# Kernel tuning notes

Hardware: AMD Instinct MI355X
Metric: run time of the kernel (lower is better)

The kernel has to match this reference:

```python
import jax, jax.numpy as jnp
import numpy as np

N_NODES = 100000
HIDDEN = 128
N_EDGES = 1000000


def setup_inputs() -> dict:
    key = jax.random.key(0)
    k1, k2, k3 = jax.random.split(key, 3)
    z = jax.random.normal(k1, (N_NODES, HIDDEN), dtype=jnp.float32)
    edge_index = jax.random.randint(k2, (2, N_EDGES), 0, N_NODES, dtype=jnp.int64)
    # xavier_uniform for square matrix: bound = sqrt(6/(fan_in+fan_out))
    bound = float(np.sqrt(6.0 / (HIDDEN + HIDDEN)))
    weights = jax.random.uniform(k3, (HIDDEN, HIDDEN), dtype=jnp.float32,
                                 minval=-bound, maxval=bound)
    return {"z": z, "edge_index": edge_index, "weights": weights}


def reference(z, edge_index, weights):
    # symm=True: symmetrize the bilinear form
    W = weights + weights.T                      # [d, d]
    z_src = z[edge_index[0]]                     # [E, d] gather
    z_dst = z[edge_index[1]]                     # [E, d] gather
    # torch: (W @ z_dst.T).T == z_dst @ W.T
    value = jnp.einsum('ed,dk,ek->e', z_src, W, z_dst)  # row-wise bilinear score
    return jax.nn.sigmoid(value)
```

## Files before the change

kernel.cpp:

```cpp
#include <hip/hip_runtime.h>

#define HIDDEN 128
#define LDSW 136
#define BSHIFT 10
#define NBMAX 128
#define CAP 10752
#define OVF_MAX 65536

typedef _Float16 f16;
typedef f16 f16x2 __attribute__((ext_vector_type(2)));
typedef f16 f16x8 __attribute__((ext_vector_type(8)));
typedef float f32x16 __attribute__((ext_vector_type(16)));
typedef unsigned long long ull;

static __device__ __forceinline__ float fdot2(f16x2 a, f16x2 b, float c) {
    return __builtin_amdgcn_fdot2(a, b, c, false);
}

__global__ __launch_bounds__(256) void prep_w(const float* __restrict__ w,
                                              f16* __restrict__ wsh_t,
                                              int* __restrict__ cursor,
                                              int* __restrict__ ovf_cnt) {
    int idx = blockIdx.x * 256 + threadIdx.x;
    if (idx < NBMAX) cursor[idx] = idx * CAP;
    if (idx == NBMAX) ovf_cnt[0] = 0;
    int n = idx >> 7, k = idx & 127;
    wsh_t[idx] = (f16)(w[k * HIDDEN + n] + w[n * HIDDEN + k]);
}

__global__ __launch_bounds__(256) void gemm_scatter(const float* __restrict__ z,
                                                    const f16* __restrict__ wsh_t,
                                                    f16* __restrict__ zh,
                                                    f16* __restrict__ uh,
                                                    const int* __restrict__ eidx,
                                                    int* __restrict__ cursor,
                                                    ull* __restrict__ perm,
                                                    ull* __restrict__ ovf,
                                                    int* __restrict__ ovf_cnt,
                                                    int nrows, int E, int nb, int ngemm) {
    __shared__ f16 wlt[HIDDEN * LDSW];
    int tid = threadIdx.x;

    if (blockIdx.x >= ngemm) {
        int* lh    = (int*)wlt;
        int* lbase = lh + NBMAX;
        int* lrank = lbase + NBMAX;
        int base = (blockIdx.x - ngemm) * 4096;
        if (tid < NBMAX) { lh[tid] = 0; lrank[tid] = 0; }
        __syncthreads();
        int s[16], d[16], bb[16];
        #pragma unroll
        for (int i = 0; i < 16; ++i) {
            int e = base + i * 256 + tid;
            bb[i] = -1;
            if (e < E) {
                s[i] = eidx[e]; d[i] = eidx[E + e];
                bb[i] = d[i] >> BSHIFT;
                atomicAdd(&lh[bb[i]], 1);
            }
        }
        __syncthreads();
        if (tid < nb && lh[tid]) lbase[tid] = atomicAdd(&cursor[tid], lh[tid]);
        __syncthreads();
        #pragma unroll
        for (int i = 0; i < 16; ++i) {
            if (bb[i] >= 0) {
                int e = base + i * 256 + tid;
                int r = atomicAdd(&lrank[bb[i]], 1);
                long pos = (long)lbase[bb[i]] + r;
                ull v = (ull)s[i] | ((ull)d[i] << 17) | ((ull)e << 34);
                if (pos < (long)(bb[i] + 1) * CAP) perm[pos] = v;
                else {
                    int o = atomicAdd(ovf_cnt, 1);
                    if (o < OVF_MAX) ovf[o] = v;
                }
            }
        }
        return;
    }

    {
        const f16x8* g = (const f16x8*)wsh_t;
        #pragma unroll
        for (int it = 0; it < 8; ++it) {
            int idx = it * 256 + tid;
            int j = idx >> 4, kc = idx & 15;
            *(f16x8*)&wlt[j * LDSW + kc * 8] = g[idx];
        }
    }
    __syncthreads();

    int wave = tid >> 6, lane = tid & 63;
    int row0 = blockIdx.x * 128 + wave * 32;
    if (row0 > nrows - 32) row0 = nrows - 32;

    int m = lane & 31, half = lane >> 5;
    const float* zr = z  + (size_t)(row0 + m) * HIDDEN + half * 8;
    f16*        zhr = zh + (size_t)(row0 + m) * HIDDEN + half * 8;
    const f16* wbase = &wlt[m * LDSW + half * 8];

    f32x16 acc0, acc1, acc2, acc3;
    #pragma unroll
    for (int r = 0; r < 16; ++r) { acc0[r] = 0.f; acc1[r] = 0.f; acc2[r] = 0.f; acc3[r] = 0.f; }

    #pragma unroll
    for (int ks = 0; ks < 8; ++ks) {
        float4 a0 = *(const float4*)(zr + 16 * ks);
        float4 a1 = *(const float4*)(zr + 16 * ks + 4);
        f16x8 af = {(f16)a0.x, (f16)a0.y, (f16)a0.z, (f16)a0.w,
                    (f16)a1.x, (f16)a1.y, (f16)a1.z, (f16)a1.w};
        *(f16x8*)(zhr + 16 * ks) = af;
        f16x8 b0 = *(const f16x8*)(wbase + 16 * ks);
        f16x8 b1 = *(const f16x8*)(wbase + 32 * LDSW + 16 * ks);
        f16x8 b2 = *(const f16x8*)(wbase + 64 * LDSW + 16 * ks);
        f16x8 b3 = *(const f16x8*)(wbase + 96 * LDSW + 16 * ks);
        acc0 = __builtin_amdgcn_mfma_f32_32x32x16_f16(af, b0, acc0, 0, 0, 0);
        acc1 = __builtin_amdgcn_mfma_f32_32x32x16_f16(af, b1, acc1, 0, 0, 0);
        acc2 = __builtin_amdgcn_mfma_f32_32x32x16_f16(af, b2, acc2, 0, 0, 0);
        acc3 = __builtin_amdgcn_mfma_f32_32x32x16_f16(af, b3, acc3, 0, 0, 0);
    }

    f16* ur = uh + (size_t)row0 * HIDDEN;
    #pragma unroll
    for (int r = 0; r < 16; ++r) {
        int row = (r & 3) + 8 * (r >> 2) + 4 * half;
        f16* p = ur + (size_t)row * HIDDEN + m;
        p[0]  = (f16)acc0[r];
        p[32] = (f16)acc1[r];
        p[64] = (f16)acc2[r];
        p[96] = (f16)acc3[r];
    }
}

static __device__ __forceinline__ void score_edge(const f16* uh, const f16* zh,
                                                  ull p, float* out, int t, int E) {
    int src = (int)(p & 0x1FFFF);
    int dst = (int)((p >> 17) & 0x1FFFF);
    int eid = (int)(p >> 34);
    const float4* a4 = (const float4*)(uh + (size_t)src * HIDDEN);
    const float4* b4 = (const float4*)(zh + (size_t)dst * HIDDEN);
    float4 av = a4[t], bv = b4[t];
    const f16x2* ap = (const f16x2*)&av;
    const f16x2* bp = (const f16x2*)&bv;
    float s = 0.f;
    #pragma unroll
    for (int i = 0; i < 4; ++i) s = fdot2(ap[i], bp[i], s);
    #pragma unroll
    for (int off = 8; off > 0; off >>= 1) s += __shfl_down(s, off, 16);
    if (t == 0 && eid < E) out[eid] = 1.0f / (1.0f + __expf(-s));
}

__global__ __launch_bounds__(256) void edge_bin(const f16* __restrict__ uh,
                                                const f16* __restrict__ zh,
                                                const ull* __restrict__ perm,
                                                const ull* __restrict__ ovf,
                                                const int* __restrict__ ovf_cnt,
                                                float* __restrict__ out,
                                                int E, int cpx, int nmain) {
    int tid = threadIdx.x;
    int g = tid >> 4, t = tid & 15;
    int b = blockIdx.x;
    if (b >= nmain) {
        int n = ovf_cnt[0];
        if (n > OVF_MAX) n = OVF_MAX;
        for (int i = (b - nmain) * 16 + g; i < n; i += 32 * 16)
            score_edge(uh, zh, ovf[i], out, t, E);
        return;
    }
    int chunk = (b & 7) * cpx + (b >> 3);
    long slot = (long)chunk * 16 + g;
    score_edge(uh, zh, perm[slot], out, t, E);
}

__global__ __launch_bounds__(256) void edge_score16(const f16* __restrict__ uh,
                                                    const f16* __restrict__ zh,
                                                    const int* __restrict__ eidx,
                                                    float* __restrict__ out, int E) {
    int tid = threadIdx.x;
    int g = tid >> 4, t = tid & 15;
    int e = blockIdx.x * 16 + g;
    if (e >= E) return;
    ull p = (ull)eidx[e] | ((ull)eidx[E + e] << 17) | ((ull)e << 34);
    score_edge(uh, zh, p, out, t, E);
}

extern "C" void kernel_launch(void* const* d_in, const int* in_sizes, int n_in,
                              void* d_out, int out_size, void* d_ws, size_t ws_size,
                              hipStream_t stream) {
    const float* z    = (const float*)d_in[0];
    const int*   eidx = (const int*)d_in[1];
    const float* w    = (const float*)d_in[2];
    float* out = (float*)d_out;

    int nrows = in_sizes[0] / HIDDEN;
    int E = out_size;
    int nb = (nrows >> BSHIFT) + 1;

    f16* wsh_t  = (f16*)d_ws;
    f16* zh     = wsh_t + HIDDEN * HIDDEN;
    f16* uh     = zh + (size_t)nrows * HIDDEN;
    int* cursor = (int*)(uh + (size_t)nrows * HIDDEN);
    int* ovf_cnt = cursor + NBMAX;
    ull* ovf    = (ull*)(ovf_cnt + 2);
    ull* perm   = ovf + OVF_MAX;

    long nslots = (long)nb * CAP;
    size_t need = (size_t)((char*)(perm + nslots) - (char*)d_ws);
    bool binned = ws_size >= need;

    int ngemm = (nrows + 127) / 128;
    int nscat = (E + 4095) / 4096;

    prep_w<<<64, 256, 0, stream>>>(w, wsh_t, cursor, ovf_cnt);
    if (binned) {
        gemm_scatter<<<ngemm + nscat, 256, 0, stream>>>(z, wsh_t, zh, uh, eidx, cursor,
                                                        perm, ovf, ovf_cnt, nrows, E, nb, ngemm);
        long ngrp = nslots / 16;
        int cpx = (int)(ngrp / 8);
        int nmain = (int)ngrp;
        edge_bin<<<nmain + 32, 256, 0, stream>>>(uh, zh, perm, ovf, ovf_cnt, out, E, cpx, nmain);
    } else {
        gemm_scatter<<<ngemm, 256, 0, stream>>>(z, wsh_t, zh, uh, eidx, cursor,
                                                perm, ovf, ovf_cnt, nrows, E, nb, ngemm);
        edge_score16<<<(E + 15) / 16, 256, 0, stream>>>(uh, zh, eidx, out, E);
    }
}
```

Baseline: 165.9 us.

## Use fine-grained 32-row destination bins with one block per bin

Shrinks the destination bins from 1024 rows to 32 rows, giving about 3.1k bins of 448 slots each. Each bin is now scored by a single 1024-thread block that loops over its slots, with bins spread across XCD-interleaved block indices. The goal is to keep each bin's small destination row set hot in cache during the gathers. In exchange, every scatter block does far more global cursor atomics and LDS histogram initialisation, and each bin's unused padding slots are still processed.

New measurement: 178.4 us. 1.08x slower.

```diff
diff --git a/kernel.cpp b/kernel.cpp
--- a/kernel.cpp
+++ b/kernel.cpp
@@ -2,10 +2,10 @@
 
 #define HIDDEN 128
 #define LDSW 136
-#define BSHIFT 10
-#define NBMAX 128
-#define CAP 10752
-#define OVF_MAX 65536
+#define BSHIFT 5
+#define NBMAX 3136
+#define CAP 448
+#define OVF_MAX 16384
 
 typedef _Float16 f16;
 typedef f16 f16x2 __attribute__((ext_vector_type(2)));
@@ -20,10 +20,11 @@
 __global__ __launch_bounds__(256) void prep_w(const float* __restrict__ w,
                                               f16* __restrict__ wsh_t,
                                               int* __restrict__ cursor,
-                                              int* __restrict__ ovf_cnt) {
+                                              int* __restrict__ ovf_cnt,
+                                              int nb) {
     int idx = blockIdx.x * 256 + threadIdx.x;
-    if (idx < NBMAX) cursor[idx] = idx * CAP;
-    if (idx == NBMAX) ovf_cnt[0] = 0;
+    if (idx < nb) cursor[idx] = idx * CAP;
+    if (idx == nb) ovf_cnt[0] = 0;
     int n = idx >> 7, k = idx & 127;
     wsh_t[idx] = (f16)(w[k * HIDDEN + n] + w[n * HIDDEN + k]);
 }
@@ -38,15 +39,15 @@
                                                     ull* __restrict__ ovf,
                                                     int* __restrict__ ovf_cnt,
                                                     int nrows, int E, int nb, int ngemm) {
-    __shared__ f16 wlt[HIDDEN * LDSW];
+    __shared__ __align__(16) char smem[3 * NBMAX * 4];
     int tid = threadIdx.x;
 
     if (blockIdx.x >= ngemm) {
-        int* lh    = (int*)wlt;
+        int* lh    = (int*)smem;
         int* lbase = lh + NBMAX;
         int* lrank = lbase + NBMAX;
         int base = (blockIdx.x - ngemm) * 4096;
-        if (tid < NBMAX) { lh[tid] = 0; lrank[tid] = 0; }
+        for (int i = tid; i < nb; i += 256) { lh[i] = 0; lrank[i] = 0; }
         __syncthreads();
         int s[16], d[16], bb[16];
         #pragma unroll
@@ -60,7 +61,8 @@
             }
         }
         __syncthreads();
-        if (tid < nb && lh[tid]) lbase[tid] = atomicAdd(&cursor[tid], lh[tid]);
+        for (int i = tid; i < nb; i += 256)
+            if (lh[i]) lbase[i] = atomicAdd(&cursor[i], lh[i]);
         __syncthreads();
         #pragma unroll
         for (int i = 0; i < 16; ++i) {
@@ -79,6 +81,7 @@
         return;
     }
 
+    f16* wlt = (f16*)smem;
     {
         const f16x8* g = (const f16x8*)wsh_t;
         #pragma unroll
@@ -150,26 +153,29 @@
     if (t == 0 && eid < E) out[eid] = 1.0f / (1.0f + __expf(-s));
 }
 
-__global__ __launch_bounds__(256) void edge_bin(const f16* __restrict__ uh,
-                                                const f16* __restrict__ zh,
-                                                const ull* __restrict__ perm,
-                                                const ull* __restrict__ ovf,
-                                                const int* __restrict__ ovf_cnt,
-                                                float* __restrict__ out,
-                                                int E, int cpx, int nmain) {
+__global__ __launch_bounds__(1024) void edge_bin(const f16* __restrict__ uh,
+                                                 const f16* __restrict__ zh,
+                                                 const ull* __restrict__ perm,
+                                                 const ull* __restrict__ ovf,
+                                                 const int* __restrict__ ovf_cnt,
+                                                 float* __restrict__ out,
+                                                 int E, int cpb, int nb, int nmain) {
     int tid = threadIdx.x;
     int g = tid >> 4, t = tid & 15;
     int b = blockIdx.x;
     if (b >= nmain) {
         int n = ovf_cnt[0];
         if (n > OVF_MAX) n = OVF_MAX;
-        for (int i = (b - nmain) * 16 + g; i < n; i += 32 * 16)
+        for (int i = (b - nmain) * 64 + g; i < n; i += 32 * 64)
             score_edge(uh, zh, ovf[i], out, t, E);
         return;
     }
-    int chunk = (b & 7) * cpx + (b >> 3);
-    long slot = (long)chunk * 16 + g;
-    score_edge(uh, zh, perm[slot], out, t, E);
+    int B = (b & 7) * cpb + (b >> 3);
+    if (B >= nb) return;
+    long base = (long)B * CAP;
+    #pragma unroll 2
+    for (int j = 0; j < CAP / 64; ++j)
+        score_edge(uh, zh, perm[base + (long)j * 64 + g], out, t, E);
 }
 
 __global__ __launch_bounds__(256) void edge_score16(const f16* __restrict__ uh,
@@ -194,7 +200,7 @@
 
     int nrows = in_sizes[0] / HIDDEN;
     int E = out_size;
-    int nb = (nrows >> BSHIFT) + 1;
+    int nb = ((nrows - 1) >> BSHIFT) + 1;
 
     f16* wsh_t  = (f16*)d_ws;
     f16* zh     = wsh_t + HIDDEN * HIDDEN;
@@ -211,14 +217,14 @@
     int ngemm = (nrows + 127) / 128;
     int nscat = (E + 4095) / 4096;
 
-    prep_w<<<64, 256, 0, stream>>>(w, wsh_t, cursor, ovf_cnt);
+    prep_w<<<64, 256, 0, stream>>>(w, wsh_t, cursor, ovf_cnt, nb);
     if (binned) {
         gemm_scatter<<<ngemm + nscat, 256, 0, stream>>>(z, wsh_t, zh, uh, eidx, cursor,
                                                         perm, ovf, ovf_cnt, nrows, E, nb, ngemm);
-        long ngrp = nslots / 16;
-        int cpx = (int)(ngrp / 8);
-        int nmain = (int)ngrp;
-        edge_bin<<<nmain + 32, 256, 0, stream>>>(uh, zh, perm, ovf, ovf_cnt, out, E, cpx, nmain);
+        int cpb = (nb + 7) / 8;
+        int nmain = 8 * cpb;
+        edge_bin<<<nmain + 32, 1024, 0, stream>>>(uh, zh, perm, ovf, ovf_cnt, out,
+                                                  E, cpb, nb, nmain);
     } else {
         gemm_scatter<<<ngemm, 256, 0, stream>>>(z, wsh_t, zh, uh, eidx, cursor,
                                                 perm, ovf, ovf_cnt, nrows, E, nb, ngemm);
```

## Drop LDS staging of W and split GEMM output columns across waves

Applied to the files above, without the earlier changes.

The GEMM part no longer copies the 128x128 f16 weight matrix into shared memory. Each block now handles 32 rows, and each of its four waves computes one 32-column slice, reading W fragments straight from global memory, which should mostly hit cache. Removing the large LDS allocation and adding a minimum-occupancy launch bound should allow more resident blocks and give the fused scatter blocks more room. The cost is four times more GEMM blocks, each wave reloading the z rows, and W being read from global/L2 instead of LDS.

After: 200.5 us. +20.9%, slower.

```diff
diff --git a/kernel.cpp b/kernel.cpp
--- a/kernel.cpp
+++ b/kernel.cpp
@@ -1,7 +1,6 @@
 #include <hip/hip_runtime.h>
 
 #define HIDDEN 128
-#define LDSW 136
 #define BSHIFT 10
 #define NBMAX 128
 #define CAP 10752
@@ -28,23 +27,20 @@
     wsh_t[idx] = (f16)(w[k * HIDDEN + n] + w[n * HIDDEN + k]);
 }
 
-__global__ __launch_bounds__(256) void gemm_scatter(const float* __restrict__ z,
-                                                    const f16* __restrict__ wsh_t,
-                                                    f16* __restrict__ zh,
-                                                    f16* __restrict__ uh,
-                                                    const int* __restrict__ eidx,
-                                                    int* __restrict__ cursor,
-                                                    ull* __restrict__ perm,
-                                                    ull* __restrict__ ovf,
-                                                    int* __restrict__ ovf_cnt,
-                                                    int nrows, int E, int nb, int ngemm) {
-    __shared__ f16 wlt[HIDDEN * LDSW];
+__global__ __launch_bounds__(256, 6) void gemm_scatter(const float* __restrict__ z,
+                                                       const f16* __restrict__ wsh_t,
+                                                       f16* __restrict__ zh,
+                                                       f16* __restrict__ uh,
+                                                       const int* __restrict__ eidx,
+                                                       int* __restrict__ cursor,
+                                                       ull* __restrict__ perm,
+                                                       ull* __restrict__ ovf,
+                                                       int* __restrict__ ovf_cnt,
+                                                       int nrows, int E, int nb, int ngemm) {
     int tid = threadIdx.x;
 
     if (blockIdx.x >= ngemm) {
-        int* lh    = (int*)wlt;
-        int* lbase = lh + NBMAX;
-        int* lrank = lbase + NBMAX;
+        __shared__ int lh[NBMAX], lbase[NBMAX], lrank[NBMAX];
         int base = (blockIdx.x - ngemm) * 4096;
         if (tid < NBMAX) { lh[tid] = 0; lrank[tid] = 0; }
         __syncthreads();
@@ -79,29 +75,18 @@
         return;
     }
 
-    {
-        const f16x8* g = (const f16x8*)wsh_t;
-        #pragma unroll
-        for (int it = 0; it < 8; ++it) {
-            int idx = it * 256 + tid;
-            int j = idx >> 4, kc = idx & 15;
-            *(f16x8*)&wlt[j * LDSW + kc * 8] = g[idx];
-        }
-    }
-    __syncthreads();
-
     int wave = tid >> 6, lane = tid & 63;
-    int row0 = blockIdx.x * 128 + wave * 32;
+    int row0 = blockIdx.x * 32;
     if (row0 > nrows - 32) row0 = nrows - 32;
 
     int m = lane & 31, half = lane >> 5;
     const float* zr = z  + (size_t)(row0 + m) * HIDDEN + half * 8;
     f16*        zhr = zh + (size_t)(row0 + m) * HIDDEN + half * 8;
-    const f16* wbase = &wlt[m * LDSW + half * 8];
-
-    f32x16 acc0, acc1, acc2, acc3;
-    #pragma unroll
-    for (int r = 0; r < 16; ++r) { acc0[r] = 0.f; acc1[r] = 0.f; acc2[r] = 0.f; acc3[r] = 0.f; }
+    const f16* wb = wsh_t + (size_t)(32 * wave + m) * HIDDEN + half * 8;
+
+    f32x16 acc;
+    #pragma unroll
+    for (int r = 0; r < 16; ++r) acc[r] = 0.f;
 
     #pragma unroll
     for (int ks = 0; ks < 8; ++ks) {
@@ -109,26 +94,16 @@
         float4 a1 = *(const float4*)(zr + 16 * ks + 4);
         f16x8 af = {(f16)a0.x, (f16)a0.y, (f16)a0.z, (f16)a0.w,
                     (f16)a1.x, (f16)a1.y, (f16)a1.z, (f16)a1.w};
-        *(f16x8*)(zhr + 16 * ks) = af;
-        f16x8 b0 = *(const f16x8*)(wbase + 16 * ks);
-        f16x8 b1 = *(const f16x8*)(wbase + 32 * LDSW + 16 * ks);
-        f16x8 b2 = *(const f16x8*)(wbase + 64 * LDSW + 16 * ks);
-        f16x8 b3 = *(const f16x8*)(wbase + 96 * LDSW + 16 * ks);
-        acc0 = __builtin_amdgcn_mfma_f32_32x32x16_f16(af, b0, acc0, 0, 0, 0);
-        acc1 = __builtin_amdgcn_mfma_f32_32x32x16_f16(af, b1, acc1, 0, 0, 0);
-        acc2 = __builtin_amdgcn_mfma_f32_32x32x16_f16(af, b2, acc2, 0, 0, 0);
-        acc3 = __builtin_amdgcn_mfma_f32_32x32x16_f16(af, b3, acc3, 0, 0, 0);
-    }
-
-    f16* ur = uh + (size_t)row0 * HIDDEN;
+        if (wave == 0) *(f16x8*)(zhr + 16 * ks) = af;
+        f16x8 b = *(const f16x8*)(wb + 16 * ks);
+        acc = __builtin_amdgcn_mfma_f32_32x32x16_f16(af, b, acc, 0, 0, 0);
+    }
+
+    f16* ur = uh + (size_t)row0 * HIDDEN + 32 * wave;
     #pragma unroll
     for (int r = 0; r < 16; ++r) {
         int row = (r & 3) + 8 * (r >> 2) + 4 * half;
-        f16* p = ur + (size_t)row * HIDDEN + m;
-        p[0]  = (f16)acc0[r];
-        p[32] = (f16)acc1[r];
-        p[64] = (f16)acc2[r];
-        p[96] = (f16)acc3[r];
+        ur[(size_t)row * HIDDEN + m] = (f16)acc[r];
     }
 }
 
@@ -208,7 +183,7 @@
     size_t need = (size_t)((char*)(perm + nslots) - (char*)d_ws);
     bool binned = ws_size >= need;
 
-    int ngemm = (nrows + 127) / 128;
+    int ngemm = (nrows + 31) / 32;
     int nscat = (E + 4095) / 4096;
 
     prep_w<<<64, 256, 0, stream>>>(w, wsh_t, cursor, ovf_cnt);
```
